# Kernel optimization log

Hardware: AMD Instinct MI355X
Metric: run time of the kernel (lower is better)

The kernel has to match this reference:

```python
import jax, jax.numpy as jnp
import numpy as np

CCA_W, INTRA_W, AUX_W, OS_W, RFS_W = 0.1, 0.05, 1.0, 1.0, 1.0


def cox_loss(risk, events, times):
    # Efron-tied Cox partial likelihood, vectorized over tie groups.
    order = jnp.argsort(-times)  # descending time
    r = risk[order]
    e = events[order]
    t = times[order]
    B = r.shape[0]
    max_r = jnp.max(r)
    exp_r = jnp.exp(r - max_r)
    cum = jnp.cumsum(exp_r)  # risk-set sums (descending time => cumsum)
    # contiguous tie groups (times sorted, ties adjacent)
    new_grp = jnp.concatenate([jnp.zeros(1, jnp.int32), (t[1:] != t[:-1]).astype(jnp.int32)])
    gid = jnp.cumsum(new_grp)
    rss = jax.ops.segment_max(cum, gid, num_segments=B)[gid]          # cum_exp_risk at last idx of group
    tes = jax.ops.segment_sum(exp_r * e, gid, num_segments=B)[gid]     # tied exp-risk sum
    d = jax.ops.segment_sum(e, gid, num_segments=B)[gid]               # tie count (events)
    # rank l of each event within its tie group (0..d-1)
    c = jnp.cumsum(e)
    start = jax.ops.segment_min(jnp.arange(B), gid, num_segments=B)[gid]
    before = c[start] - e[start]
    l = c - 1.0 - before
    d_safe = jnp.where(d > 0, d, 1.0)
    denom = rss - (l / d_safe) * tes
    contrib = e * (r - jnp.log(denom + 1e-12) - max_r)
    n_events = jnp.sum(e)
    return -jnp.sum(contrib) / (n_events + 1e-12)


def distance_correlation_loss(za, zb):
    def dist(x):
        xx = jnp.sum(x * x, axis=1, keepdims=True)
        d2 = xx + xx.T - 2.0 * (x @ x.T)
        return jnp.sqrt(jnp.maximum(d2, 1e-8))
    def dc(D):
        return D - D.mean(axis=1, keepdims=True) - D.mean(axis=0, keepdims=True) + D.mean()
    A = dc(dist(za))
    Bm = dc(dist(zb))
    dcov = jnp.mean(A * Bm)
    va = jnp.mean(A * A)
    vb = jnp.mean(Bm * Bm)
    return 1.0 - dcov / jnp.sqrt(jnp.maximum(va * vb, 1e-8))


def setup_inputs() -> dict:
    key = jax.random.key(0)
    ks = jax.random.split(key, 10)
    B, D = 8192, 256
    return {
        'risk_os': jax.random.normal(ks[0], (B,), jnp.float32),
        'risk_rfs': jax.random.normal(ks[1], (B,), jnp.float32),
        'z_ct': jax.random.normal(ks[2], (B, D), jnp.float32),
        'z_wsi': jax.random.normal(ks[3], (B, D), jnp.float32),
        'intra_wsi': jax.random.uniform(ks[4], (), jnp.float32),
        'intra_ct': jax.random.uniform(ks[5], (), jnp.float32),
        'evt_os': jax.random.randint(ks[6], (B,), 0, 2, jnp.int32),
        'tm_os': jax.random.randint(ks[7], (B,), 0, 1000, jnp.int32),
        'evt_rfs': jax.random.randint(ks[8], (B,), 0, 2, jnp.int32),
        'tm_rfs': jax.random.randint(ks[9], (B,), 0, 1000, jnp.int32),
    }


def reference(risk_os, risk_rfs, z_ct, z_wsi, intra_wsi, intra_ct,
              evt_os, tm_os, evt_rfs, tm_rfs):
    l_os = cox_loss(risk_os, evt_os.astype(jnp.float32), tm_os.astype(jnp.float32))
    l_rfs = cox_loss(risk_rfs, evt_rfs.astype(jnp.float32), tm_rfs.astype(jnp.float32))
    l_cca = distance_correlation_loss(z_ct, z_wsi)
    l_intra = intra_wsi + intra_ct
    total = OS_W * l_os + RFS_W * l_rfs + AUX_W * (CCA_W * l_cca + INTRA_W * l_intra)
    return total
```

## Files before the change

### kernel.cpp

```cpp
#include <hip/hip_runtime.h>
#include <hip/hip_bf16.h>
#include <math.h>

typedef __attribute__((ext_vector_type(4))) float f32x4;
typedef __attribute__((ext_vector_type(4))) int int4v;

#define NBINS 1000

__device__ __forceinline__ void gl16(const void* g, void* l) {
  __builtin_amdgcn_global_load_lds(
      (const __attribute__((address_space(1))) unsigned int*)g,
      (__attribute__((address_space(3))) unsigned int*)l, 16, 0, 0);
}

__device__ __forceinline__ float fp8mag(unsigned b) {
  const int e = (b >> 3) & 15;
  const int m = b & 7;
  return e ? ldexpf((float)(8 + m), e - 10) : ldexpf((float)m, -9);
}

__global__ __launch_bounds__(256)
void prep_kernel(const float* __restrict__ za, const float* __restrict__ zb,
                 float* __restrict__ na, float* __restrict__ nb,
                 unsigned char* __restrict__ zpa, unsigned char* __restrict__ zpb,
                 int B, int D)
{
  const int row = blockIdx.x * 4 + (threadIdx.x >> 6);
  const int lane = threadIdx.x & 63;
  const float* src; float* dst; unsigned char* bd; int r;
  if (row < B) { src = za; dst = na; bd = zpa; r = row; }
  else         { src = zb; dst = nb; bd = zpb; r = row - B; }
  const int rr = r & 127;
  const int sw = (rr >> 1) & 3;
  const size_t tbase = (size_t)(r >> 7) * 128 * D;
  float s = 0.f;
  for (int c = lane * 4; c < D; c += 256) {
    const f32x4 v = *(const f32x4*)&src[(size_t)r * D + c];
    unsigned u = (unsigned)__builtin_amdgcn_cvt_pk_fp8_f32(v[0], v[1], 0, false);
    u = (unsigned)__builtin_amdgcn_cvt_pk_fp8_f32(v[2], v[3], (int)u, true);
    const int sc = c >> 6;
    const int half = (c >> 5) & 1;
    const int kg = (c >> 3) & 3;
    const int rem = c & 7;
    const int slot = kg ^ sw;
    *(unsigned*)&bd[tbase + sc * 8192 + rr * 64 + slot * 16 + half * 8 + rem] = u;
    const float x0 = fp8mag(u & 255), x1 = fp8mag((u >> 8) & 255);
    const float x2 = fp8mag((u >> 16) & 255), x3 = fp8mag(u >> 24);
    s += x0 * x0 + x1 * x1 + x2 * x2 + x3 * x3;
  }
#pragma unroll
  for (int off = 32; off; off >>= 1) s += __shfl_xor(s, off);
  if (lane == 0) dst[r] = s;
}

__global__ __launch_bounds__(512, 2)
void dcor_kernel(const unsigned char* __restrict__ zpa,
                 const unsigned char* __restrict__ zpb,
                 const float* __restrict__ na, const float* __restrict__ nb,
                 float* __restrict__ Ra, float* __restrict__ Rb,
                 double* __restrict__ scalPart,
                 const float* __restrict__ r0, const int* __restrict__ e0, const int* __restrict__ t0,
                 const float* __restrict__ r1, const int* __restrict__ e1, const int* __restrict__ t1,
                 float* __restrict__ coxo,
                 int nt, int B, int D)
{
  __shared__ __align__(16) union SU {
    unsigned char jbuf[3][16384];
    struct { float sS[NBINS], sT[NBINS], sDc[NBINS], sc0[NBINS], sc1[NBINS], red[16], red3[48]; } c;
  } u;

  const int tid = threadIdx.x;
  const int bid = blockIdx.x;

  if (bid < 2) {
    const float* risk = bid ? r1 : r0;
    const int* evt = bid ? e1 : e0;
    const int* tm  = bid ? t1 : t0;
    const int NT = 512;

    float m = -3.0e38f;
    for (int i = tid; i < B; i += NT) m = fmaxf(m, risk[i]);
#pragma unroll
    for (int off = 32; off; off >>= 1) m = fmaxf(m, __shfl_xor(m, off));
    if ((tid & 63) == 0) u.c.red[tid >> 6] = m;
    __syncthreads();
    if (tid == 0) {
      float mm = u.c.red[0];
      for (int wv = 1; wv < 8; ++wv) mm = fmaxf(mm, u.c.red[wv]);
      u.c.red[0] = mm;
    }
    __syncthreads();
    const float maxr = u.c.red[0];

    for (int i = tid; i < NBINS; i += NT) { u.c.sS[i] = 0.f; u.c.sT[i] = 0.f; u.c.sDc[i] = 0.f; }
    __syncthreads();

    float sr = 0.f, nev = 0.f;
    for (int i = tid; i < B; i += NT) {
      const float r = risk[i];
      int t = tm[i];
      t = t < 0 ? 0 : (t >= NBINS ? NBINS - 1 : t);
      const float ex = expf(r - maxr);
      atomicAdd(&u.c.sS[t], ex);
      if (evt[i]) {
        atomicAdd(&u.c.sT[t], ex);
        atomicAdd(&u.c.sDc[t], 1.0f);
        sr += r; nev += 1.0f;
      }
    }
    __syncthreads();

    for (int i = tid; i < NBINS; i += NT) u.c.sc0[i] = u.c.sS[i];
    __syncthreads();
    float* pin = u.c.sc0; float* pout = u.c.sc1;
    for (int off = 1; off < NBINS; off <<= 1) {
      for (int i = tid; i < NBINS; i += NT) {
        float v = pin[i];
        if (i + off < NBINS) v += pin[i + off];
        pout[i] = v;
      }
      __syncthreads();
      float* tmp = pin; pin = pout; pout = tmp;
    }

    float ls = 0.f;
    for (int t = tid; t < NBINS; t += NT) {
      const float d = u.c.sDc[t];
      if (d > 0.f) {
        const float tes = u.c.sT[t];
        const float rs = pin[t];
        for (float l = 0.f; l < d - 0.5f; l += 1.f)
          ls += logf(rs - (l / d) * tes + 1e-12f);
      }
    }

    float v1 = sr, v2 = nev, v3 = ls;
#pragma unroll
    for (int off = 32; off; off >>= 1) {
      v1 += __shfl_xor(v1, off); v2 += __shfl_xor(v2, off); v3 += __shfl_xor(v3, off);
    }
    if ((tid & 63) == 0) { int wv = tid >> 6; u.c.red3[wv] = v1; u.c.red3[16 + wv] = v2; u.c.red3[32 + wv] = v3; }
    __syncthreads();
    if (tid == 0) {
      float SR = 0.f, NEV = 0.f, LS = 0.f;
      for (int wv = 0; wv < 8; ++wv) { SR += u.c.red3[wv]; NEV += u.c.red3[16 + wv]; LS += u.c.red3[32 + wv]; }
      coxo[bid] = -(SR - LS - NEV * maxr) / (NEV + 1e-12f);
    }
    return;
  }

  const int lane = tid & 63;
  const int w = tid >> 6;
  const int p = bid - 2;

  const int xcd = p & 7, pos = p >> 3;
  const int q = (xcd < 6 ? xcd * 32 : 192 + (xcd - 6) * 31) + pos;
  const int start = (q < 48) ? 9 * q : 432 + 8 * (q - 48);
  const int cnt = (q < 48) ? 9 : 8;

  const double tn = (double)(2 * nt + 1);
  int ib0 = (int)((tn - sqrt(tn * tn - 8.0 * (double)start)) * 0.5);
  if (ib0 < 0) ib0 = 0;
  if (ib0 > nt - 1) ib0 = nt - 1;
  while (((ib0 + 1) * nt - ((ib0 + 1) * ib0) / 2) <= start) ++ib0;
  while ((ib0 * nt - (ib0 * (ib0 - 1)) / 2) > start) --ib0;
  const int jb0 = ib0 + (start - (ib0 * nt - (ib0 * (ib0 - 1)) / 2));

  const int wr = w >> 1, wc = w & 1;
  const int lrow = lane & 15;
  const int kg = lane >> 4;
  const int kgx = kg ^ ((lrow >> 1) & 3);
  const int abase = (wr * 32 + lrow) * 64 + kgx * 16;
  const int bbase = (wc * 64 + lrow) * 64 + kgx * 16;

  union I4L { int4v v; long l[2]; };

  int cib = ib0, cjb = jb0;
  int ssib = ib0, ssjb = jb0;
  const unsigned char* pAi = zpa + (size_t)cib * 32768;
  const unsigned char* pBi = zpb + (size_t)cib * 32768;
  const unsigned char* sAj = zpa + (size_t)ssjb * 32768;
  const unsigned char* sBj = zpb + (size_t)ssjb * 32768;

  I4L iA[2][4], iB[2][4];
#pragma unroll
  for (int m2 = 0; m2 < 2; ++m2)
#pragma unroll
    for (int sc = 0; sc < 4; ++sc) {
      iA[m2][sc].v = *(const int4v*)(pAi + sc * 8192 + abase + m2 * 1024);
      iB[m2][sc].v = *(const int4v*)(pBi + sc * 8192 + abase + m2 * 1024);
    }

  const int lgofs = w * 1024 + lane * 16;
  const int llofs = w * 1024;

  const f32x4 Z4 = {0.f, 0.f, 0.f, 0.f};
  f32x4 accA[2][4], accB[2][4];
#pragma unroll
  for (int m2 = 0; m2 < 2; ++m2)
#pragma unroll
    for (int n2 = 0; n2 < 4; ++n2) { accA[m2][n2] = Z4; accB[m2][n2] = Z4; }

  double dp0 = 0.0, dp1 = 0.0, dp2 = 0.0;

  gl16(sAj + 0 * 8192 + lgofs, &u.jbuf[0][llofs]);
  gl16(sBj + 0 * 8192 + lgofs, &u.jbuf[0][8192 + llofs]);
  gl16(sAj + 1 * 8192 + lgofs, &u.jbuf[1][llofs]);
  gl16(sBj + 1 * 8192 + lgofs, &u.jbuf[1][8192 + llofs]);

  int bufc = 0;
  int bufs = 2;

  for (int t = 0; t < cnt; ++t) {
#pragma unroll
    for (int sc = 0; sc < 4; ++sc) {
      if (t == cnt - 1 && sc == 3) asm volatile("s_waitcnt vmcnt(0)" ::: "memory");
      else                         asm volatile("s_waitcnt vmcnt(2)" ::: "memory");
      __builtin_amdgcn_sched_barrier(0);
      __builtin_amdgcn_s_barrier();
      __builtin_amdgcn_sched_barrier(0);

      if (t + 1 < cnt || sc < 2) {
        if (sc == 2) {
          if (++ssjb == nt) { ++ssib; ssjb = ssib; }
          sAj = zpa + (size_t)ssjb * 32768;
          sBj = zpb + (size_t)ssjb * 32768;
        }
        const size_t co = (size_t)((sc + 2) & 3) * 8192 + lgofs;
        gl16(sAj + co, &u.jbuf[bufs][llofs]);
        gl16(sBj + co, &u.jbuf[bufs][8192 + llofs]);
      }

      {
        const unsigned char* jb_ = &u.jbuf[bufc][0];
        I4L bA[4], bB[4];
#pragma unroll
        for (int n2 = 0; n2 < 4; ++n2) bA[n2].v = *(const int4v*)&jb_[bbase + n2 * 1024];
#pragma unroll
        for (int n2 = 0; n2 < 4; ++n2) bB[n2].v = *(const int4v*)&jb_[8192 + bbase + n2 * 1024];
        __builtin_amdgcn_s_setprio(1);
#pragma unroll
        for (int m2 = 0; m2 < 2; ++m2)
#pragma unroll
          for (int n2 = 0; n2 < 4; ++n2) {
            accA[m2][n2] = __builtin_amdgcn_mfma_f32_16x16x32_fp8_fp8(iA[m2][sc].l[0], bA[n2].l[0], accA[m2][n2], 0, 0, 0);
            accA[m2][n2] = __builtin_amdgcn_mfma_f32_16x16x32_fp8_fp8(iA[m2][sc].l[1], bA[n2].l[1], accA[m2][n2], 0, 0, 0);
          }
#pragma unroll
        for (int m2 = 0; m2 < 2; ++m2)
#pragma unroll
          for (int n2 = 0; n2 < 4; ++n2) {
            accB[m2][n2] = __builtin_amdgcn_mfma_f32_16x16x32_fp8_fp8(iB[m2][sc].l[0], bB[n2].l[0], accB[m2][n2], 0, 0, 0);
            accB[m2][n2] = __builtin_amdgcn_mfma_f32_16x16x32_fp8_fp8(iB[m2][sc].l[1], bB[n2].l[1], accB[m2][n2], 0, 0, 0);
          }
        __builtin_amdgcn_s_setprio(0);
      }

      bufc = (bufc == 2) ? 0 : bufc + 1;
      bufs = (bufs == 2) ? 0 : bufs + 1;
    }

    {
      const bool offd = (cjb != cib);
      const float fac = offd ? 2.0f : 1.0f;
      float pab = 0.f, paa = 0.f, pbb = 0.f;
      float rsa[2][4], rsb[2][4];
      float csa[4] = {0.f, 0.f, 0.f, 0.f}, csb[4] = {0.f, 0.f, 0.f, 0.f};
#pragma unroll
      for (int m2 = 0; m2 < 2; ++m2)
#pragma unroll
        for (int r = 0; r < 4; ++r) { rsa[m2][r] = 0.f; rsb[m2][r] = 0.f; }

      const int gi0 = cib * 128 + wr * 32;
      const int gj0 = cjb * 128 + wc * 64;

#pragma unroll
      for (int m2 = 0; m2 < 2; ++m2) {
        const int gr = gi0 + m2 * 16 + kg * 4;
        const f32x4 nai = *(const f32x4*)&na[gr];
        const f32x4 nbi = *(const f32x4*)&nb[gr];
#pragma unroll
        for (int n2 = 0; n2 < 4; ++n2) {
          const int gc = gj0 + n2 * 16 + lrow;
          const float naj = na[gc];
          const float nbj = nb[gc];
          const f32x4 ga = accA[m2][n2];
          const f32x4 gb = accB[m2][n2];
#pragma unroll
          for (int r = 0; r < 4; ++r) {
            const float d2a = fmaxf(nai[r] + naj - 2.0f * ga[r], 1e-8f);
            const float d2b = fmaxf(nbi[r] + nbj - 2.0f * gb[r], 1e-8f);
            const float Da = __builtin_amdgcn_sqrtf(d2a);
            const float Db = __builtin_amdgcn_sqrtf(d2b);
            pab += Da * Db;
            paa += d2a;
            pbb += d2b;
            rsa[m2][r] += Da;
            rsb[m2][r] += Db;
            csa[n2] += Da;
            csb[n2] += Db;
          }
        }
      }

#pragma unroll
      for (int m2 = 0; m2 < 2; ++m2)
#pragma unroll
        for (int r = 0; r < 4; ++r) {
          float va = rsa[m2][r], vb = rsb[m2][r];
          va += __shfl_xor(va, 1); va += __shfl_xor(va, 2); va += __shfl_xor(va, 4); va += __shfl_xor(va, 8);
          vb += __shfl_xor(vb, 1); vb += __shfl_xor(vb, 2); vb += __shfl_xor(vb, 4); vb += __shfl_xor(vb, 8);
          if (lrow == 0) {
            const int gi = gi0 + m2 * 16 + kg * 4 + r;
            atomicAdd(&Ra[gi], va);
            atomicAdd(&Rb[gi], vb);
          }
        }

      if (offd) {
#pragma unroll
        for (int n2 = 0; n2 < 4; ++n2) {
          float va = csa[n2], vb = csb[n2];
          va += __shfl_xor(va, 16); va += __shfl_xor(va, 32);
          vb += __shfl_xor(vb, 16); vb += __shfl_xor(vb, 32);
          if (kg == 0) {
            const int gj = gj0 + n2 * 16 + lrow;
            atomicAdd(&Ra[gj], va);
            atomicAdd(&Rb[gj], vb);
          }
        }
      }

      float q1 = fac * pab, q2 = fac * paa, q3 = fac * pbb;
#pragma unroll
      for (int off = 32; off; off >>= 1) {
        q1 += __shfl_xor(q1, off); q2 += __shfl_xor(q2, off); q3 += __shfl_xor(q3, off);
      }
      dp0 += (double)q1; dp1 += (double)q2; dp2 += (double)q3;
    }

    const int oldib = cib;
    if (++cjb == nt) { ++cib; cjb = cib; }
    if (cib != oldib && t + 1 < cnt) {
      pAi = zpa + (size_t)cib * 32768;
      pBi = zpb + (size_t)cib * 32768;
#pragma unroll
      for (int m2 = 0; m2 < 2; ++m2)
#pragma unroll
        for (int sc = 0; sc < 4; ++sc) {
          iA[m2][sc].v = *(const int4v*)(pAi + sc * 8192 + abase + m2 * 1024);
          iB[m2][sc].v = *(const int4v*)(pBi + sc * 8192 + abase + m2 * 1024);
        }
    }
#pragma unroll
    for (int m2 = 0; m2 < 2; ++m2)
#pragma unroll
      for (int n2 = 0; n2 < 4; ++n2) { accA[m2][n2] = Z4; accB[m2][n2] = Z4; }
  }

  if (lane == 0) {
    double* sp = scalPart + (size_t)(p * 8 + w) * 3;
    sp[0] = dp0; sp[1] = dp1; sp[2] = dp2;
  }
}

__global__ __launch_bounds__(256)
void finalize_kernel(const float* __restrict__ Ra, const float* __restrict__ Rb,
                     const double* __restrict__ scalPart, int NS,
                     const float* __restrict__ coxo,
                     const float* __restrict__ iw, const float* __restrict__ ic,
                     float* __restrict__ out, int B)
{
  const int tid = threadIdx.x;
  double v[8];
#pragma unroll
  for (int k = 0; k < 8; ++k) v[k] = 0.0;
  for (int i = tid; i < B; i += 256) {
    const double a = Ra[i], b = Rb[i];
    v[0] += a; v[1] += b; v[2] += a * b; v[3] += a * a; v[4] += b * b;
  }
  for (int i = tid; i < NS; i += 256) {
    const double* sp = scalPart + (size_t)i * 3;
    v[5] += sp[0]; v[6] += sp[1]; v[7] += sp[2];
  }
#pragma unroll
  for (int k = 0; k < 8; ++k)
#pragma unroll
    for (int off = 32; off; off >>= 1) v[k] += __shfl_xor(v[k], off);
  __shared__ double sred[32];
  const int w = tid >> 6;
  if ((tid & 63) == 0) {
#pragma unroll
    for (int k = 0; k < 8; ++k) sred[k * 4 + w] = v[k];
  }
  __syncthreads();
  if (tid == 0) {
    double r[8];
#pragma unroll
    for (int k = 0; k < 8; ++k) r[k] = sred[k * 4] + sred[k * 4 + 1] + sred[k * 4 + 2] + sred[k * 4 + 3];
    const double ta = r[0], tb = r[1], sab = r[2], saa = r[3], sbb = r[4];
    const double Pab = r[5], Paa = r[6], Pbb = r[7];
    const double n = (double)B;
    const double Sab = Pab - (2.0 / n) * sab + ta * tb / (n * n);
    const double Saa = Paa - (2.0 / n) * saa + ta * ta / (n * n);
    const double Sbb = Pbb - (2.0 / n) * sbb + tb * tb / (n * n);
    const double dcov = Sab / (n * n);
    const double va = Saa / (n * n);
    const double vb = Sbb / (n * n);
    const double l_cca = 1.0 - dcov / sqrt(fmax(va * vb, 1e-8));
    const double total = (double)coxo[0] + (double)coxo[1]
                       + (0.1 * l_cca + 0.05 * ((double)iw[0] + (double)ic[0]));
    out[0] = (float)total;
  }
}

extern "C" void kernel_launch(void* const* d_in, const int* in_sizes, int n_in,
                              void* d_out, int out_size, void* d_ws, size_t ws_size,
                              hipStream_t stream)
{
  (void)n_in; (void)out_size; (void)ws_size;
  const float* risk_os   = (const float*)d_in[0];
  const float* risk_rfs  = (const float*)d_in[1];
  const float* z_ct      = (const float*)d_in[2];
  const float* z_wsi     = (const float*)d_in[3];
  const float* intra_wsi = (const float*)d_in[4];
  const float* intra_ct  = (const float*)d_in[5];
  const int* evt_os  = (const int*)d_in[6];
  const int* tm_os   = (const int*)d_in[7];
  const int* evt_rfs = (const int*)d_in[8];
  const int* tm_rfs  = (const int*)d_in[9];

  const int B = in_sizes[0];
  const int D = in_sizes[2] / B;
  const int nt = B / 128;
  const int NS = 254 * 8;

  float* ws = (float*)d_ws;
  float* Ra = ws;
  float* Rb = ws + B;
  float* coxo = ws + 2 * B;
  float* na  = ws + 2 * B + 16;
  float* nbv = ws + 3 * B + 16;
  double* scalPart = (double*)(ws + 4 * B + 16);
  unsigned char* zpa = (unsigned char*)(ws + 4 * B + 16 + 6 * NS + 8);
  unsigned char* zpb = zpa + (size_t)B * D;

  (void)hipMemsetAsync(d_ws, 0, (size_t)(2 * B) * sizeof(float), stream);

  prep_kernel<<<(2 * B) / 4, 256, 0, stream>>>(z_ct, z_wsi, na, nbv, zpa, zpb, B, D);
  dcor_kernel<<<256, 512, 0, stream>>>(zpa, zpb, na, nbv, Ra, Rb, scalPart,
                                       risk_os, evt_os, tm_os, risk_rfs, evt_rfs, tm_rfs,
                                       coxo, nt, B, D);
  finalize_kernel<<<1, 256, 0, stream>>>(Ra, Rb, scalPart, NS, coxo, intra_wsi, intra_ct, (float*)d_out, B);
}
```

Baseline: 89.92 us.

## Restructure LDS pipeline to double-buffered half-tile stages, bit-cast fp8 decode

Changes the j-tile LDS staging from a triple-buffered ring of quarter K-chunks to two buffers holding two K-chunks each. That halves the number of wait-and-barrier points per tile, but adds a second barrier after compute before each refill. Each async load stage becomes larger, which could expose more load latency. It also replaces the ldexpf-based fp8 magnitude decode with direct float bit construction.

```diff
diff --git a/kernel.cpp b/kernel.cpp
--- a/kernel.cpp
+++ b/kernel.cpp
@@ -14,9 +14,11 @@
 }
 
 __device__ __forceinline__ float fp8mag(unsigned b) {
-  const int e = (b >> 3) & 15;
-  const int m = b & 7;
-  return e ? ldexpf((float)(8 + m), e - 10) : ldexpf((float)m, -9);
+  const unsigned e = (b >> 3) & 15u;
+  const unsigned m = b & 7u;
+  union { unsigned u; float f; } c;
+  c.u = ((e + 120u) << 23) | (m << 20);
+  return e ? c.f : (float)m * 0.001953125f;
 }
 
 __global__ __launch_bounds__(256)
@@ -65,7 +67,7 @@
                  int nt, int B, int D)
 {
   __shared__ __align__(16) union SU {
-    unsigned char jbuf[3][16384];
+    unsigned char jbuf[2][32768];
     struct { float sS[NBINS], sT[NBINS], sDc[NBINS], sc0[NBINS], sc1[NBINS], red[16], red3[48]; } c;
   } u;
 
@@ -194,6 +196,15 @@
   const int lgofs = w * 1024 + lane * 16;
   const int llofs = w * 1024;
 
+#define STAGE(par_, scb_) do {                                         \
+    const size_t c0_ = (size_t)(scb_) * 8192 + lgofs;                  \
+    const size_t c1_ = (size_t)((scb_) + 1) * 8192 + lgofs;            \
+    gl16(sAj + c0_, &u.jbuf[par_][llofs]);                             \
+    gl16(sAj + c1_, &u.jbuf[par_][8192 + llofs]);                      \
+    gl16(sBj + c0_, &u.jbuf[par_][16384 + llofs]);                     \
+    gl16(sBj + c1_, &u.jbuf[par_][24576 + llofs]);                     \
+  } while (0)
+
   const f32x4 Z4 = {0.f, 0.f, 0.f, 0.f};
   f32x4 accA[2][4], accB[2][4];
 #pragma unroll
@@ -203,61 +214,58 @@
 
   double dp0 = 0.0, dp1 = 0.0, dp2 = 0.0;
 
-  gl16(sAj + 0 * 8192 + lgofs, &u.jbuf[0][llofs]);
-  gl16(sBj + 0 * 8192 + lgofs, &u.jbuf[0][8192 + llofs]);
-  gl16(sAj + 1 * 8192 + lgofs, &u.jbuf[1][llofs]);
-  gl16(sBj + 1 * 8192 + lgofs, &u.jbuf[1][8192 + llofs]);
-
-  int bufc = 0;
-  int bufs = 2;
+  STAGE(0, 0);
+  STAGE(1, 2);
 
   for (int t = 0; t < cnt; ++t) {
 #pragma unroll
-    for (int sc = 0; sc < 4; ++sc) {
-      if (t == cnt - 1 && sc == 3) asm volatile("s_waitcnt vmcnt(0)" ::: "memory");
-      else                         asm volatile("s_waitcnt vmcnt(2)" ::: "memory");
+    for (int h = 0; h < 2; ++h) {
+      if (t == cnt - 1 && h == 1) asm volatile("s_waitcnt vmcnt(0)" ::: "memory");
+      else                        asm volatile("s_waitcnt vmcnt(4)" ::: "memory");
       __builtin_amdgcn_sched_barrier(0);
       __builtin_amdgcn_s_barrier();
       __builtin_amdgcn_sched_barrier(0);
 
-      if (t + 1 < cnt || sc < 2) {
-        if (sc == 2) {
+      {
+        const unsigned char* jb_ = &u.jbuf[h][0];
+#pragma unroll
+        for (int half = 0; half < 2; ++half) {
+          I4L bA[4], bB[4];
+#pragma unroll
+          for (int n2 = 0; n2 < 4; ++n2) bA[n2].v = *(const int4v*)&jb_[half * 8192 + bbase + n2 * 1024];
+#pragma unroll
+          for (int n2 = 0; n2 < 4; ++n2) bB[n2].v = *(const int4v*)&jb_[16384 + half * 8192 + bbase + n2 * 1024];
+          __builtin_amdgcn_s_setprio(1);
+#pragma unroll
+          for (int m2 = 0; m2 < 2; ++m2)
+#pragma unroll
+            for (int n2 = 0; n2 < 4; ++n2) {
+              accA[m2][n2] = __builtin_amdgcn_mfma_f32_16x16x32_fp8_fp8(iA[m2][2 * h + half].l[0], bA[n2].l[0], accA[m2][n2], 0, 0, 0);
+              accA[m2][n2] = __builtin_amdgcn_mfma_f32_16x16x32_fp8_fp8(iA[m2][2 * h + half].l[1], bA[n2].l[1], accA[m2][n2], 0, 0, 0);
+            }
+#pragma unroll
+          for (int m2 = 0; m2 < 2; ++m2)
+#pragma unroll
+            for (int n2 = 0; n2 < 4; ++n2) {
+              accB[m2][n2] = __builtin_amdgcn_mfma_f32_16x16x32_fp8_fp8(iB[m2][2 * h + half].l[0], bB[n2].l[0], accB[m2][n2], 0, 0, 0);
+              accB[m2][n2] = __builtin_amdgcn_mfma_f32_16x16x32_fp8_fp8(iB[m2][2 * h + half].l[1], bB[n2].l[1], accB[m2][n2], 0, 0, 0);
+            }
+          __builtin_amdgcn_s_setprio(0);
+        }
+      }
+
+      __builtin_amdgcn_sched_barrier(0);
+      __builtin_amdgcn_s_barrier();
+      __builtin_amdgcn_sched_barrier(0);
+
+      if (t + 1 < cnt) {
+        if (h == 0) {
           if (++ssjb == nt) { ++ssib; ssjb = ssib; }
           sAj = zpa + (size_t)ssjb * 32768;
           sBj = zpb + (size_t)ssjb * 32768;
         }
-        const size_t co = (size_t)((sc + 2) & 3) * 8192 + lgofs;
-        gl16(sAj + co, &u.jbuf[bufs][llofs]);
-        gl16(sBj + co, &u.jbuf[bufs][8192 + llofs]);
-      }
-
-      {
-        const unsigned char* jb_ = &u.jbuf[bufc][0];
-        I4L bA[4], bB[4];
-#pragma unroll
-        for (int n2 = 0; n2 < 4; ++n2) bA[n2].v = *(const int4v*)&jb_[bbase + n2 * 1024];
-#pragma unroll
-        for (int n2 = 0; n2 < 4; ++n2) bB[n2].v = *(const int4v*)&jb_[8192 + bbase + n2 * 1024];
-        __builtin_amdgcn_s_setprio(1);
-#pragma unroll
-        for (int m2 = 0; m2 < 2; ++m2)
-#pragma unroll
-          for (int n2 = 0; n2 < 4; ++n2) {
-            accA[m2][n2] = __builtin_amdgcn_mfma_f32_16x16x32_fp8_fp8(iA[m2][sc].l[0], bA[n2].l[0], accA[m2][n2], 0, 0, 0);
-            accA[m2][n2] = __builtin_amdgcn_mfma_f32_16x16x32_fp8_fp8(iA[m2][sc].l[1], bA[n2].l[1], accA[m2][n2], 0, 0, 0);
-          }
-#pragma unroll
-        for (int m2 = 0; m2 < 2; ++m2)
-#pragma unroll
-          for (int n2 = 0; n2 < 4; ++n2) {
-            accB[m2][n2] = __builtin_amdgcn_mfma_f32_16x16x32_fp8_fp8(iB[m2][sc].l[0], bB[n2].l[0], accB[m2][n2], 0, 0, 0);
-            accB[m2][n2] = __builtin_amdgcn_mfma_f32_16x16x32_fp8_fp8(iB[m2][sc].l[1], bB[n2].l[1], accB[m2][n2], 0, 0, 0);
-          }
-        __builtin_amdgcn_s_setprio(0);
-      }
-
-      bufc = (bufc == 2) ? 0 : bufc + 1;
-      bufs = (bufs == 2) ? 0 : bufs + 1;
+        STAGE(h, 2 * h);
+      }
     }
 
     {
@@ -357,6 +365,7 @@
 #pragma unroll
       for (int n2 = 0; n2 < 4; ++n2) { accA[m2][n2] = Z4; accB[m2][n2] = Z4; }
   }
+#undef STAGE
 
   if (lane == 0) {
     double* sp = scalPart + (size_t)(p * 8 + w) * 3;
```

New measurement: 90.36 us. No clear change (+0.5%).
